# Optimization experiments

Hardware: AMD Instinct MI355X
Metric: run time of the kernel (lower is better)

The kernel has to match this reference:

```python
import jax, jax.numpy as jnp
import numpy as np

N = 50000      # nodes
E = 800000     # edges (avg degree 16)
D = 96         # input_size == output_size
C = 10         # n_class
STEPS = 4      # num_layers -> GGNN propagation steps


def setup_inputs() -> dict:
    key = jax.random.key(0)
    ks = jax.random.split(key, 12)
    s = 1.0 / np.sqrt(D)
    return {
        "x": jax.random.normal(ks[0], (N, D), dtype=jnp.float32),
        "src": jax.random.randint(ks[1], (E,), 0, N, dtype=jnp.int32),
        "dst": jax.random.randint(ks[2], (E,), 0, N, dtype=jnp.int32),
        # edge message transform (DGL GatedGraphConv: Linear(out, out) per etype, 1 etype)
        "W_e": jax.random.normal(ks[3], (D, D), dtype=jnp.float32) * s,
        "b_e": jax.random.normal(ks[4], (D,), dtype=jnp.float32) * s,
        # GRUCell params (torch layout: rows ordered r, z, n)
        "W_ih": jax.random.normal(ks[5], (3 * D, D), dtype=jnp.float32) * s,
        "W_hh": jax.random.normal(ks[6], (3 * D, D), dtype=jnp.float32) * s,
        "b_ih": jax.random.normal(ks[7], (3 * D,), dtype=jnp.float32) * s,
        "b_hh": jax.random.normal(ks[8], (3 * D,), dtype=jnp.float32) * s,
        # classifier head
        "W_fc": jax.random.normal(ks[9], (C, D), dtype=jnp.float32) * s,
        "b_fc": jax.random.normal(ks[10], (C,), dtype=jnp.float32) * s,
    }


def _gru_cell(a, h, W_ih, W_hh, b_ih, b_hh):
    # torch.nn.GRUCell math; gate order r, z, n
    gx = a @ W_ih.T + b_ih            # [N, 3D]
    gh = h @ W_hh.T + b_hh            # [N, 3D]
    xr, xz, xn = jnp.split(gx, 3, axis=-1)
    hr, hz, hn = jnp.split(gh, 3, axis=-1)
    r = jax.nn.sigmoid(xr + hr)
    z = jax.nn.sigmoid(xz + hz)
    n = jnp.tanh(xn + r * hn)
    return (1.0 - z) * n + z * h


def reference(x, src, dst, W_e, b_e, W_ih, W_hh, b_ih, b_hh, W_fc, b_fc):
    h = x  # in_feats == out_feats, no padding needed
    for _ in range(STEPS):
        m = h @ W_e.T + b_e                                  # per-node transform [N, D]
        a = jax.ops.segment_sum(m[src], dst, num_segments=N) # gather + scatter-add [N, D]
        h = _gru_cell(a, h, W_ih, W_hh, b_ih, b_hh)
    logits = jax.nn.elu(h) @ W_fc.T + b_fc                   # [N, C]
    return logits
```

## Files before the change

### kernel.cpp

```cpp
#include <hip/hip_runtime.h>

static constexpr int D = 96;
static constexpr int G3 = 3 * D;
static constexpr int NSTEPS = 4;
static constexpr int NT = 18;
static constexpr int SCAN_BLK = 1024;

typedef __attribute__((ext_vector_type(8))) _Float16 f16x8;
typedef __attribute__((ext_vector_type(4))) _Float16 f16x4;
typedef __attribute__((ext_vector_type(4))) float f32x4;

__device__ __forceinline__ f16x8 load_a_frag(const _Float16* __restrict__ base,
                                             int r0, int lane, int kc) {
  int row = r0 + (lane & 15);
  int k0 = kc * 32 + ((lane >> 4) << 3);
  return *(const f16x8*)(base + (size_t)row * D + k0);
}

__device__ __forceinline__ f16x8 load_b_swz(const _Float16* __restrict__ W,
                                            int t, int kc, int lane) {
  return *(const f16x8*)(W + (((size_t)t * 3 + kc) * 64 + lane) * 8);
}


__global__ void convert_x_kernel(const float* __restrict__ x,
                                 _Float16* __restrict__ h, int total4) {
  int i = blockIdx.x * blockDim.x + threadIdx.x;
  if (i >= total4) return;
  float4 v = ((const float4*)x)[i];
  f16x4 o;
  o[0] = (_Float16)v.x; o[1] = (_Float16)v.y;
  o[2] = (_Float16)v.z; o[3] = (_Float16)v.w;
  *(f16x4*)(h + (size_t)i * 4) = o;
}

__global__ void compute_wx_kernel(const float* __restrict__ Wih,
                                  const float* __restrict__ We,
                                  const float* __restrict__ be,
                                  float* __restrict__ Wx,
                                  float* __restrict__ bxe) {
  int idx = blockIdx.x * blockDim.x + threadIdx.x;
  if (idx < G3 * D) {
    int r = idx / D, k = idx - r * D;
    float acc = 0.f;
    for (int c = 0; c < D; ++c) acc += Wih[r * D + c] * We[c * D + k];
    Wx[idx] = acc;
  } else if (idx < G3 * D + G3) {
    int r = idx - G3 * D;
    float acc = 0.f;
    for (int c = 0; c < D; ++c) acc += Wih[r * D + c] * be[c];
    bxe[r] = acc;
  }
}

__global__ void swizzle_f16_kernel(const float* __restrict__ Wx,
                                   const float* __restrict__ Whh,
                                   _Float16* __restrict__ WxF,
                                   _Float16* __restrict__ WhhF) {
  int idx = blockIdx.x * blockDim.x + threadIdx.x;
  if (idx >= 2 * NT * 3 * 64) return;
  int mat = idx / (NT * 3 * 64);
  int rem = idx - mat * (NT * 3 * 64);
  int t = rem / (3 * 64);
  int rem2 = rem - t * (3 * 64);
  int kc = rem2 >> 6;
  int lane = rem2 & 63;
  int c = t * 16 + (lane & 15);
  int k0 = kc * 32 + ((lane >> 4) << 3);
  const float* W = mat ? Whh : Wx;
  _Float16* dF = mat ? WhhF : WxF;
  f16x8 o;
#pragma unroll
  for (int j = 0; j < 8; ++j) o[j] = (_Float16)W[(size_t)c * D + k0 + j];
  *(f16x8*)(dF + (((size_t)t * 3 + kc) * 64 + lane) * 8) = o;
}


__global__ void hist_kernel(const int* __restrict__ dst, int* __restrict__ counts, int E) {
  int e = blockIdx.x * blockDim.x + threadIdx.x;
  if (e < E) atomicAdd(&counts[dst[e]], 1);
}

__global__ void partial_sum_kernel(const int* __restrict__ counts,
                                   int* __restrict__ blk_sums, int n) {
  __shared__ int red[256];
  int base = blockIdx.x * SCAN_BLK;
  int tid = threadIdx.x;
  int s = 0;
#pragma unroll
  for (int j = 0; j < 4; ++j) {
    int i = base + j * 256 + tid;
    if (i < n) s += counts[i];
  }
  red[tid] = s;
  __syncthreads();
  for (int off = 128; off > 0; off >>= 1) {
    if (tid < off) red[tid] += red[tid + off];
    __syncthreads();
  }
  if (tid == 0) blk_sums[blockIdx.x] = red[0];
}

__global__ void scan_offsets_kernel(const int* __restrict__ blk_sums,
                                    int* __restrict__ blk_off,
                                    int* __restrict__ row_ptr, int nb, int n) {
  __shared__ int lds[64];
  int tid = threadIdx.x;
  if (tid < nb) lds[tid] = blk_sums[tid];
  __syncthreads();
  if (tid == 0) {
    int run = 0;
    for (int i = 0; i < nb; ++i) { blk_off[i] = run; run += lds[i]; }
    row_ptr[n] = run;
  }
}

__global__ void block_scan_kernel(const int* __restrict__ counts,
                                  const int* __restrict__ blk_off,
                                  int* __restrict__ row_ptr, int n) {
  __shared__ int red[256];
  int base = blockIdx.x * SCAN_BLK;
  int tid = threadIdx.x;
  int i0 = base + tid * 4;
  int v0 = 0, v1 = 0, v2 = 0, v3 = 0;
  if (i0 + 3 < n) {
    int4 c = *(const int4*)(counts + i0);
    v0 = c.x; v1 = c.y; v2 = c.z; v3 = c.w;
  } else {
    if (i0 < n) v0 = counts[i0];
    if (i0 + 1 < n) v1 = counts[i0 + 1];
    if (i0 + 2 < n) v2 = counts[i0 + 2];
  }
  int tsum = v0 + v1 + v2 + v3;
  red[tid] = tsum;
  __syncthreads();
  for (int off = 1; off < 256; off <<= 1) {
    int t = (tid >= off) ? red[tid - off] : 0;
    __syncthreads();
    red[tid] += t;
    __syncthreads();
  }
  int excl = blk_off[blockIdx.x] + red[tid] - tsum;
  if (i0 < n) row_ptr[i0] = excl;
  if (i0 + 1 < n) row_ptr[i0 + 1] = excl + v0;
  if (i0 + 2 < n) row_ptr[i0 + 2] = excl + v0 + v1;
  if (i0 + 3 < n) row_ptr[i0 + 3] = excl + v0 + v1 + v2;
}

__global__ void fill_kernel(const int* __restrict__ src, const int* __restrict__ dst,
                            const int* __restrict__ row_ptr,
                            int* __restrict__ fillc, int* __restrict__ csr_src, int E) {
  int e = blockIdx.x * blockDim.x + threadIdx.x;
  if (e >= E) return;
  int t = dst[e];
  int pos = row_ptr[t] + atomicAdd(&fillc[t], 1);
  __builtin_nontemporal_store(src[e], &csr_src[pos]);
}


__global__ void aggregate_kernel(const _Float16* __restrict__ h,
                                 const int* __restrict__ row_ptr,
                                 const int* __restrict__ csr_src,
                                 _Float16* __restrict__ s, int n) {
  int tid = blockIdx.x * blockDim.x + threadIdx.x;
  int i = tid / 12;
  int c8 = tid - i * 12;
  if (i >= n) return;
  int beg = row_ptr[i], end = row_ptr[i + 1];
  float acc[8] = {0.f, 0.f, 0.f, 0.f, 0.f, 0.f, 0.f, 0.f};
  int e = beg;
  for (; e + 3 < end; e += 4) {
    int s0 = csr_src[e], s1 = csr_src[e + 1], s2 = csr_src[e + 2], s3 = csr_src[e + 3];
    f16x8 v0 = *(const f16x8*)(h + (size_t)s0 * D + c8 * 8);
    f16x8 v1 = *(const f16x8*)(h + (size_t)s1 * D + c8 * 8);
    f16x8 v2 = *(const f16x8*)(h + (size_t)s2 * D + c8 * 8);
    f16x8 v3 = *(const f16x8*)(h + (size_t)s3 * D + c8 * 8);
#pragma unroll
    for (int j = 0; j < 8; ++j)
      acc[j] += (float)v0[j] + (float)v1[j] + ((float)v2[j] + (float)v3[j]);
  }
  for (; e < end; ++e) {
    f16x8 v = *(const f16x8*)(h + (size_t)csr_src[e] * D + c8 * 8);
#pragma unroll
    for (int j = 0; j < 8; ++j) acc[j] += (float)v[j];
  }
  f16x8 out;
#pragma unroll
  for (int j = 0; j < 8; ++j) out[j] = (_Float16)acc[j];
  *(f16x8*)(s + (size_t)i * D + c8 * 8) = out;
}

__device__ __forceinline__ void store_planes(float* lds, const f32x4* accM,
                                             const f32x4* accE, int main_plane,
                                             int extra_plane, int extra_ct0, int lane) {
  int col_l = lane & 15;
  int rq = (lane >> 4) << 2;
#pragma unroll
  for (int ct = 0; ct < 6; ++ct)
#pragma unroll
    for (int q = 0; q < 4; ++q)
      lds[main_plane * (16 * D) + (rq + q) * D + ct * 16 + col_l] = accM[ct][q];
#pragma unroll
  for (int ct = 0; ct < 3; ++ct)
#pragma unroll
    for (int q = 0; q < 4; ++q)
      lds[extra_plane * (16 * D) + (rq + q) * D + (extra_ct0 + ct) * 16 + col_l] = accE[ct][q];
}

__device__ __forceinline__ void gru_epilogue(const float* lds,
                                             const _Float16* __restrict__ h,
                                             _Float16* __restrict__ hout,
                                             const int* __restrict__ row_ptr,
                                             const float* __restrict__ bxe,
                                             const float* __restrict__ bih,
                                             const float* __restrict__ bhh,
                                             int base_row, int tid) {
#pragma unroll
  for (int j = 0; j < 6; ++j) {
    int e = tid + j * 256;
    int row = e / D;
    int col = e - row * D;
    int grow = base_row + row;
    float degf = (float)(row_ptr[grow + 1] - row_ptr[grow]);
    float R  = lds[e] + lds[16 * D + e];
    float Z  = lds[2 * 16 * D + e] + lds[3 * 16 * D + e];
    float XN = lds[4 * 16 * D + e];
    float HN = lds[5 * 16 * D + e];
    float rg = 1.0f / (1.0f + __expf(-(R + bih[col] + bhh[col] + degf * bxe[col])));
    float zg = 1.0f / (1.0f + __expf(-(Z + bih[D + col] + bhh[D + col] + degf * bxe[D + col])));
    float ng = tanhf(XN + bih[2 * D + col] + degf * bxe[2 * D + col] + rg * (HN + bhh[2 * D + col]));
    float hv = (float)h[(size_t)grow * D + col];
    hout[(size_t)grow * D + col] = (_Float16)((1.0f - zg) * ng + zg * hv);
  }
}

__global__ __launch_bounds__(256) void gru_gemm_kernel(
    const _Float16* __restrict__ s, const _Float16* __restrict__ h,
    _Float16* __restrict__ hout, const int* __restrict__ row_ptr,
    const _Float16* __restrict__ WxF, const _Float16* __restrict__ WhhF,
    const float* __restrict__ bxe, const float* __restrict__ bih,
    const float* __restrict__ bhh, int n) {
  __shared__ float lds[6 * 16 * D];
  int r0 = blockIdx.x << 5;
  int w = threadIdx.x >> 6;
  int lane = threadIdx.x & 63;

  const int opS = (w < 2) ? 1 : 0;
  const _Float16* A = opS ? s : h;
  const _Float16* WF = opS ? WxF : WhhF;
  const int half = w & 1;
  const int main_t0 = half * 6;
  const int main_plane = half * 2 + (opS ? 0 : 1);
  const int extra_t0 = 12 + half * 3;
  const int extra_ct0 = half * 3;
  const int extra_plane = opS ? 4 : 5;

  f16x8 a0[3], a1[3];
#pragma unroll
  for (int kc = 0; kc < 3; ++kc) {
    a0[kc] = load_a_frag(A, r0, lane, kc);
    a1[kc] = load_a_frag(A, r0 + 16, lane, kc);
  }

  f32x4 accM0[6], accM1[6], accE0[3], accE1[3];
#pragma unroll
  for (int t = 0; t < 6; ++t) {
    accM0[t] = (f32x4){0.f, 0.f, 0.f, 0.f};
    accM1[t] = (f32x4){0.f, 0.f, 0.f, 0.f};
  }
#pragma unroll
  for (int t = 0; t < 3; ++t) {
    accE0[t] = (f32x4){0.f, 0.f, 0.f, 0.f};
    accE1[t] = (f32x4){0.f, 0.f, 0.f, 0.f};
  }

#pragma unroll
  for (int ct = 0; ct < 6; ++ct)
#pragma unroll
    for (int kc = 0; kc < 3; ++kc) {
      f16x8 b = load_b_swz(WF, main_t0 + ct, kc, lane);
      accM0[ct] = __builtin_amdgcn_mfma_f32_16x16x32_f16(a0[kc], b, accM0[ct], 0, 0, 0);
      accM1[ct] = __builtin_amdgcn_mfma_f32_16x16x32_f16(a1[kc], b, accM1[ct], 0, 0, 0);
    }
#pragma unroll
  for (int ct = 0; ct < 3; ++ct)
#pragma unroll
    for (int kc = 0; kc < 3; ++kc) {
      f16x8 b = load_b_swz(WF, extra_t0 + ct, kc, lane);
      accE0[ct] = __builtin_amdgcn_mfma_f32_16x16x32_f16(a0[kc], b, accE0[ct], 0, 0, 0);
      accE1[ct] = __builtin_amdgcn_mfma_f32_16x16x32_f16(a1[kc], b, accE1[ct], 0, 0, 0);
    }

  store_planes(lds, accM0, accE0, main_plane, extra_plane, extra_ct0, lane);
  __syncthreads();
  gru_epilogue(lds, h, hout, row_ptr, bxe, bih, bhh, r0, threadIdx.x);
  __syncthreads();
  if (r0 + 16 < n) {
    store_planes(lds, accM1, accE1, main_plane, extra_plane, extra_ct0, lane);
    __syncthreads();
    gru_epilogue(lds, h, hout, row_ptr, bxe, bih, bhh, r0 + 16, threadIdx.x);
  }
}

__global__ void head_kernel(const _Float16* __restrict__ h,
                            const float* __restrict__ Wfc,
                            const float* __restrict__ bfc,
                            float* __restrict__ out,
                            int n, int C) {
  int idx = blockIdx.x * blockDim.x + threadIdx.x;
  if (idx >= n * C) return;
  int i = idx / C;
  int c = idx - i * C;
  const _Float16* hr = h + (size_t)i * D;
  const float* wr = Wfc + (size_t)c * D;
  float acc = bfc[c];
#pragma unroll 8
  for (int k = 0; k < D; ++k) {
    float hv = (float)hr[k];
    float e = hv > 0.0f ? hv : (__expf(hv) - 1.0f);
    acc += e * wr[k];
  }
  out[idx] = acc;
}

extern "C" void kernel_launch(void* const* d_in, const int* in_sizes, int n_in,
                              void* d_out, int out_size, void* d_ws, size_t ws_size,
                              hipStream_t stream) {
  const float* x    = (const float*)d_in[0];
  const int*   src  = (const int*)d_in[1];
  const int*   dst  = (const int*)d_in[2];
  const float* W_e  = (const float*)d_in[3];
  const float* b_e  = (const float*)d_in[4];
  const float* W_ih = (const float*)d_in[5];
  const float* W_hh = (const float*)d_in[6];
  const float* b_ih = (const float*)d_in[7];
  const float* b_hh = (const float*)d_in[8];
  const float* W_fc = (const float*)d_in[9];
  const float* b_fc = (const float*)d_in[10];

  const int n = in_sizes[0] / D;
  const int E = in_sizes[1];
  const int C = out_size / n;

  _Float16* hA = (_Float16*)d_ws;
  _Float16* hB = hA + (size_t)n * D;
  _Float16* s  = hB + (size_t)n * D;
  float* Wx    = (float*)(s + (size_t)n * D);
  _Float16* WxF  = (_Float16*)(Wx + (size_t)G3 * D);
  _Float16* WhhF = WxF + (size_t)G3 * D;
  float* bxe   = (float*)(WhhF + (size_t)G3 * D);
  int* counts  = (int*)(bxe + G3);
  int* fillc   = counts + n;
  int* row_ptr = fillc + n;
  int* csr_src = row_ptr + (n + 1);
  int* blk_sums = csr_src + E;
  int* blk_off  = blk_sums + 64;

  const int threads = 256;
  const int nb = (n + SCAN_BLK - 1) / SCAN_BLK;

  (void)hipMemsetAsync(counts, 0, (size_t)2 * n * sizeof(int), stream);
  hist_kernel<<<(E + threads - 1) / threads, threads, 0, stream>>>(dst, counts, E);
  partial_sum_kernel<<<nb, 256, 0, stream>>>(counts, blk_sums, n);
  scan_offsets_kernel<<<1, 64, 0, stream>>>(blk_sums, blk_off, row_ptr, nb, n);
  block_scan_kernel<<<nb, 256, 0, stream>>>(counts, blk_off, row_ptr, n);
  fill_kernel<<<(E + threads - 1) / threads, threads, 0, stream>>>(src, dst, row_ptr,
                                                                   fillc, csr_src, E);
  compute_wx_kernel<<<(G3 * D + G3 + threads - 1) / threads, threads, 0, stream>>>(
      W_ih, W_e, b_e, Wx, bxe);
  swizzle_f16_kernel<<<(2 * NT * 3 * 64 + threads - 1) / threads, threads, 0, stream>>>(
      Wx, W_hh, WxF, WhhF);
  convert_x_kernel<<<((n * D / 4) + threads - 1) / threads, threads, 0, stream>>>(
      x, hA, n * D / 4);

  const int gridAgg = (int)(((size_t)n * 12 + threads - 1) / threads);
  const int gridG = (n + 31) / 32;

  const _Float16* hcur = hA;
  _Float16* hnext = hB;
  for (int step = 0; step < NSTEPS; ++step) {
    aggregate_kernel<<<gridAgg, threads, 0, stream>>>(hcur, row_ptr, csr_src, s, n);
    gru_gemm_kernel<<<gridG, threads, 0, stream>>>(s, hcur, hnext, row_ptr,
                                                   WxF, WhhF, bxe, b_ih, b_hh, n);
    const _Float16* t = hcur; hcur = hnext; hnext = (_Float16*)t;
  }

  const int gridH = (n * C + threads - 1) / threads;
  head_kernel<<<gridH, threads, 0, stream>>>(hcur, W_fc, b_fc, (float*)d_out, n, C);
}
```

Measured before the change: 370.8 us.

## Fuse neighbor aggregation into GRU GEMM kernel via shared-memory staging

Removes the separate aggregate kernel and the global buffer for aggregated features. Each GRU block now gathers and sums neighbor rows for its 32 nodes into a padded shared-memory tile, then feeds the MFMA A-fragments for the input-gate GEMM straight from LDS. This drops one launch per step and one global round trip of the N×D aggregate. The trade-off is that the gather now uses 8 threads per row with narrower 4-wide loads, and the GEMM waves must wait for all gathering before starting. The CSR fill also switches from a nontemporal store to a plain store.

```diff
diff --git a/kernel.cpp b/kernel.cpp
--- a/kernel.cpp
+++ b/kernel.cpp
@@ -5,6 +5,7 @@
 static constexpr int NSTEPS = 4;
 static constexpr int NT = 18;
 static constexpr int SCAN_BLK = 1024;
+static constexpr int SLP = 104;
 
 typedef __attribute__((ext_vector_type(8))) _Float16 f16x8;
 typedef __attribute__((ext_vector_type(4))) _Float16 f16x4;
@@ -154,41 +155,9 @@
   if (e >= E) return;
   int t = dst[e];
   int pos = row_ptr[t] + atomicAdd(&fillc[t], 1);
-  __builtin_nontemporal_store(src[e], &csr_src[pos]);
-}
-
-
-__global__ void aggregate_kernel(const _Float16* __restrict__ h,
-                                 const int* __restrict__ row_ptr,
-                                 const int* __restrict__ csr_src,
-                                 _Float16* __restrict__ s, int n) {
-  int tid = blockIdx.x * blockDim.x + threadIdx.x;
-  int i = tid / 12;
-  int c8 = tid - i * 12;
-  if (i >= n) return;
-  int beg = row_ptr[i], end = row_ptr[i + 1];
-  float acc[8] = {0.f, 0.f, 0.f, 0.f, 0.f, 0.f, 0.f, 0.f};
-  int e = beg;
-  for (; e + 3 < end; e += 4) {
-    int s0 = csr_src[e], s1 = csr_src[e + 1], s2 = csr_src[e + 2], s3 = csr_src[e + 3];
-    f16x8 v0 = *(const f16x8*)(h + (size_t)s0 * D + c8 * 8);
-    f16x8 v1 = *(const f16x8*)(h + (size_t)s1 * D + c8 * 8);
-    f16x8 v2 = *(const f16x8*)(h + (size_t)s2 * D + c8 * 8);
-    f16x8 v3 = *(const f16x8*)(h + (size_t)s3 * D + c8 * 8);
-#pragma unroll
-    for (int j = 0; j < 8; ++j)
-      acc[j] += (float)v0[j] + (float)v1[j] + ((float)v2[j] + (float)v3[j]);
-  }
-  for (; e < end; ++e) {
-    f16x8 v = *(const f16x8*)(h + (size_t)csr_src[e] * D + c8 * 8);
-#pragma unroll
-    for (int j = 0; j < 8; ++j) acc[j] += (float)v[j];
-  }
-  f16x8 out;
-#pragma unroll
-  for (int j = 0; j < 8; ++j) out[j] = (_Float16)acc[j];
-  *(f16x8*)(s + (size_t)i * D + c8 * 8) = out;
-}
+  csr_src[pos] = src[e];
+}
+
 
 __device__ __forceinline__ void store_planes(float* lds, const f32x4* accM,
                                              const f32x4* accE, int main_plane,
@@ -234,19 +203,61 @@
   }
 }
 
-__global__ __launch_bounds__(256) void gru_gemm_kernel(
-    const _Float16* __restrict__ s, const _Float16* __restrict__ h,
-    _Float16* __restrict__ hout, const int* __restrict__ row_ptr,
+__global__ __launch_bounds__(256) void gru_fused_kernel(
+    const _Float16* __restrict__ h, _Float16* __restrict__ hout,
+    const int* __restrict__ row_ptr, const int* __restrict__ csr_src,
     const _Float16* __restrict__ WxF, const _Float16* __restrict__ WhhF,
     const float* __restrict__ bxe, const float* __restrict__ bih,
     const float* __restrict__ bhh, int n) {
   __shared__ float lds[6 * 16 * D];
+  __shared__ _Float16 sl[32][SLP];
   int r0 = blockIdx.x << 5;
   int w = threadIdx.x >> 6;
   int lane = threadIdx.x & 63;
 
+  {
+    int row = threadIdx.x >> 3;
+    int part = threadIdx.x & 7;
+    int grow = r0 + row;
+    float acc[12];
+#pragma unroll
+    for (int j = 0; j < 12; ++j) acc[j] = 0.f;
+    if (grow < n) {
+      int beg = row_ptr[grow], end = row_ptr[grow + 1];
+      int e = beg;
+      for (; e + 1 < end; e += 2) {
+        const _Float16* p0 = h + (size_t)csr_src[e] * D + part * 12;
+        const _Float16* p1 = h + (size_t)csr_src[e + 1] * D + part * 12;
+        f16x4 u0 = *(const f16x4*)(p0), u1 = *(const f16x4*)(p0 + 4), u2 = *(const f16x4*)(p0 + 8);
+        f16x4 v0 = *(const f16x4*)(p1), v1 = *(const f16x4*)(p1 + 4), v2 = *(const f16x4*)(p1 + 8);
+#pragma unroll
+        for (int j = 0; j < 4; ++j) {
+          acc[j]     += (float)u0[j] + (float)v0[j];
+          acc[4 + j] += (float)u1[j] + (float)v1[j];
+          acc[8 + j] += (float)u2[j] + (float)v2[j];
+        }
+      }
+      if (e < end) {
+        const _Float16* p0 = h + (size_t)csr_src[e] * D + part * 12;
+        f16x4 u0 = *(const f16x4*)(p0), u1 = *(const f16x4*)(p0 + 4), u2 = *(const f16x4*)(p0 + 8);
+#pragma unroll
+        for (int j = 0; j < 4; ++j) {
+          acc[j] += (float)u0[j]; acc[4 + j] += (float)u1[j]; acc[8 + j] += (float)u2[j];
+        }
+      }
+    }
+    f16x4 o0, o1, o2;
+#pragma unroll
+    for (int j = 0; j < 4; ++j) {
+      o0[j] = (_Float16)acc[j]; o1[j] = (_Float16)acc[4 + j]; o2[j] = (_Float16)acc[8 + j];
+    }
+    *(f16x4*)&sl[row][part * 12]     = o0;
+    *(f16x4*)&sl[row][part * 12 + 4] = o1;
+    *(f16x4*)&sl[row][part * 12 + 8] = o2;
+  }
+  __syncthreads();
+
   const int opS = (w < 2) ? 1 : 0;
-  const _Float16* A = opS ? s : h;
   const _Float16* WF = opS ? WxF : WhhF;
   const int half = w & 1;
   const int main_t0 = half * 6;
@@ -256,10 +267,19 @@
   const int extra_plane = opS ? 4 : 5;
 
   f16x8 a0[3], a1[3];
-#pragma unroll
-  for (int kc = 0; kc < 3; ++kc) {
-    a0[kc] = load_a_frag(A, r0, lane, kc);
-    a1[kc] = load_a_frag(A, r0 + 16, lane, kc);
+  if (opS) {
+#pragma unroll
+    for (int kc = 0; kc < 3; ++kc) {
+      int k0 = kc * 32 + ((lane >> 4) << 3);
+      a0[kc] = *(const f16x8*)&sl[lane & 15][k0];
+      a1[kc] = *(const f16x8*)&sl[16 + (lane & 15)][k0];
+    }
+  } else {
+#pragma unroll
+    for (int kc = 0; kc < 3; ++kc) {
+      a0[kc] = load_a_frag(h, r0, lane, kc);
+      a1[kc] = load_a_frag(h, r0 + 16, lane, kc);
+    }
   }
 
   f32x4 accM0[6], accM1[6], accE0[3], accE1[3];
@@ -291,6 +311,7 @@
       accE1[ct] = __builtin_amdgcn_mfma_f32_16x16x32_f16(a1[kc], b, accE1[ct], 0, 0, 0);
     }
 
+  __syncthreads();
   store_planes(lds, accM0, accE0, main_plane, extra_plane, extra_ct0, lane);
   __syncthreads();
   gru_epilogue(lds, h, hout, row_ptr, bxe, bih, bhh, r0, threadIdx.x);
@@ -344,8 +365,7 @@
 
   _Float16* hA = (_Float16*)d_ws;
   _Float16* hB = hA + (size_t)n * D;
-  _Float16* s  = hB + (size_t)n * D;
-  float* Wx    = (float*)(s + (size_t)n * D);
+  float* Wx    = (float*)(hB + (size_t)n * D);
   _Float16* WxF  = (_Float16*)(Wx + (size_t)G3 * D);
   _Float16* WhhF = WxF + (size_t)G3 * D;
   float* bxe   = (float*)(WhhF + (size_t)G3 * D);
@@ -373,15 +393,13 @@
   convert_x_kernel<<<((n * D / 4) + threads - 1) / threads, threads, 0, stream>>>(
       x, hA, n * D / 4);
 
-  const int gridAgg = (int)(((size_t)n * 12 + threads - 1) / threads);
   const int gridG = (n + 31) / 32;
 
   const _Float16* hcur = hA;
   _Float16* hnext = hB;
   for (int step = 0; step < NSTEPS; ++step) {
-    aggregate_kernel<<<gridAgg, threads, 0, stream>>>(hcur, row_ptr, csr_src, s, n);
-    gru_gemm_kernel<<<gridG, threads, 0, stream>>>(s, hcur, hnext, row_ptr,
-                                                   WxF, WhhF, bxe, b_ih, b_hh, n);
+    gru_fused_kernel<<<gridG, threads, 0, stream>>>(hcur, hnext, row_ptr, csr_src,
+                                                    WxF, WhhF, bxe, b_ih, b_hh, n);
     const _Float16* t = hcur; hcur = hnext; hnext = (_Float16*)t;
   }
 
```

Result: faster. 362.6 us (-2.2%).
